# Kernel tuning notes

Measured on AMD Instinct MI355X. Metric: run time of the kernel, lower is better.

The kernel has to match this reference:

```python
import jax, jax.numpy as jnp
import numpy as np

DIM = 512
NUM_HEADS = 8
HEAD_DIM = DIM // NUM_HEADS
GAMMA = 1.0


def setup_inputs() -> dict:
    key = jax.random.key(0)
    ks = jax.random.split(key, 10)
    B, S = 2, 2048
    x_real = jax.random.normal(ks[0], (B, S, DIM), dtype=jnp.float32)
    x_imag = jax.random.normal(ks[1], (B, S, DIM), dtype=jnp.float32)
    def xavier(k, fan_in, fan_out):
        lim = float(np.sqrt(6.0 / (fan_in + fan_out)))
        return jax.random.uniform(k, (fan_in, fan_out), jnp.float32, -lim, lim)
    # torch Linear(in,out): weight [out,in]; we store transposed [in,out]
    Wq = xavier(ks[2], 2 * DIM, DIM); bq = jnp.zeros((DIM,), jnp.float32)
    Wk = xavier(ks[3], 2 * DIM, DIM); bk = jnp.zeros((DIM,), jnp.float32)
    Wv = xavier(ks[4], 2 * DIM, DIM); bv = jnp.zeros((DIM,), jnp.float32)
    Wo = xavier(ks[5], DIM, 2 * DIM); bo = jnp.zeros((2 * DIM,), jnp.float32)
    return {"x_real": x_real, "x_imag": x_imag, "Wq": Wq, "bq": bq,
            "Wk": Wk, "bk": bk, "Wv": Wv, "bv": bv, "Wo": Wo, "bo": bo}


def reference(x_real, x_imag, Wq, bq, Wk, bk, Wv, bv, Wo, bo):
    B, S, _ = x_real.shape
    real_embed = jnp.concatenate([x_real, x_imag], axis=-1)  # [B,S,2*dim]
    def proj(W, b):
        y = real_embed @ W + b                               # [B,S,dim]
        return y.reshape(B, S, NUM_HEADS, HEAD_DIM).transpose(0, 2, 1, 3)  # [B,H,S,d]
    Q = proj(Wq, bq)
    K = proj(Wk, bk)
    V = proj(Wv, bv)
    # softmax over head_dim is broadcast-invariant, so the Bhattacharyya
    # coefficient sum_d sqrt(p_i[d]*q_j[d]) factorizes into a matmul.
    sp = jnp.sqrt(jax.nn.softmax(Q, axis=-1))  # [B,H,S,d]
    sq = jnp.sqrt(jax.nn.softmax(K, axis=-1))  # [B,H,S,d]
    bc = jnp.einsum('bhid,bhjd->bhij', sp, sq)  # Bhattacharyya coeff [B,H,S,S]
    bc = jnp.clip(bc, -1.0, 1.0)
    dist = jnp.arccos(bc)
    attn = jax.nn.softmax(-GAMMA * dist * dist, axis=-1)  # [B,H,S,S]
    attended = jnp.einsum('bhij,bhjd->bhid', attn, V)
    attended = attended.transpose(0, 2, 1, 3).reshape(B, S, DIM)
    out = attended @ Wo + bo  # [B,S,2*dim] = concat(real_out, imag_out)
    return out
```

## Files before the change

kernel.cpp:

```cpp
#include <hip/hip_runtime.h>
#include <math.h>


typedef __attribute__((ext_vector_type(8))) short short8;
typedef __attribute__((ext_vector_type(4))) short bf16x4;
typedef __attribute__((ext_vector_type(4))) float f32x4;
typedef __attribute__((ext_vector_type(2))) float f32x2;
typedef __attribute__((ext_vector_type(4))) unsigned int u32x4;

#define MFMA(a, b, c) __builtin_amdgcn_mfma_f32_16x16x32_bf16((a), (b), (c), 0, 0, 0)

static __device__ __forceinline__ short f2bf(float f) {
    unsigned u = __float_as_uint(f);
    u += 0x7fffu + ((u >> 16) & 1u);
    return (short)(u >> 16);
}

static __device__ __forceinline__ void gld_lds16(const short* g, short* l) {
    __builtin_amdgcn_global_load_lds(
        (const __attribute__((address_space(1))) unsigned int*)g,
        (__attribute__((address_space(3))) unsigned int*)l, 16, 0, 0);
}

__global__ __launch_bounds__(256) void prep_all(
    const float* __restrict__ xr, const float* __restrict__ xi,
    short* __restrict__ xb,
    const float* __restrict__ Wq, const float* __restrict__ Wk,
    const float* __restrict__ Wv, const float* __restrict__ Wo,
    short* __restrict__ wqt, short* __restrict__ wot)
{
    const int bid = blockIdx.x;
    if (bid < 2048) {
        const unsigned wid = bid * 256 + threadIdx.x;
        const int p  = wid & 7;
        const int rp = (wid >> 3) & 31;
        const int kt = (wid >> 8) & 31;
        const int mb = wid >> 13;
        const int up = p ^ (rp & 7);
        const int m  = (mb << 6) | (rp << 1) | (up >> 2);
        const int k  = (kt << 5) | ((up & 3) << 3);
        const float* s = (k < 512) ? (xr + (size_t)m * 512 + k)
                                   : (xi + (size_t)m * 512 + (k - 512));
        float4 t0 = *(const float4*)(s);
        float4 t1 = *(const float4*)(s + 4);
        short8 o;
        o[0] = f2bf(t0.x); o[1] = f2bf(t0.y); o[2] = f2bf(t0.z); o[3] = f2bf(t0.w);
        o[4] = f2bf(t1.x); o[5] = f2bf(t1.y); o[6] = f2bf(t1.z); o[7] = f2bf(t1.w);
        *(short8*)(xb + (size_t)wid * 8) = o;
    } else {
        __shared__ float tt[32][33];
        const int t = bid - 2048;
        const int z = t >> 9;
        const int idx = t & 511;
        const float* src = (z == 0) ? Wq : (z == 1) ? Wk : (z == 2) ? Wv : Wo;
        const int N = (z < 3) ? 512 : 1024;
        const int bx = (z < 3) ? (idx & 15) : (idx & 31);
        const int by = (z < 3) ? (idx >> 4) : (idx >> 5);
        const int n0 = bx << 5, k0 = by << 5;
        const int tx = threadIdx.x & 31, ty = threadIdx.x >> 5;
        #pragma unroll
        for (int i = 0; i < 4; ++i)
            tt[ty + 8 * i][tx] = src[(size_t)(k0 + ty + 8 * i) * N + n0 + tx];
        __syncthreads();
        const int k = k0 + tx;
        const int kt = k >> 5, u = (k >> 3) & 3, off = k & 7;
        #pragma unroll
        for (int i = 0; i < 4; ++i) {
            const int n = n0 + ty + 8 * i;
            const int nb = n >> 6, rn = n & 63;
            const int rp = rn >> 1;
            const int up = ((rn & 1) << 2) | u;
            const int p  = up ^ (rp & 7);
            const float v = tt[tx][ty + 8 * i];
            if (z < 3)
                wqt[(size_t)z * 524288 +
                    ((size_t)(nb * 32 + kt)) * 2048 + rp * 64 + p * 8 + off] = f2bf(v);
            else
                wot[((size_t)(nb * 16 + kt)) * 2048 + rp * 64 + p * 8 + off] = f2bf(v);
        }
    }
}

__global__ __launch_bounds__(64) void qkv_mfma(
    const short* __restrict__ xb, const short* __restrict__ wcat,
    const float* __restrict__ bq, const float* __restrict__ bk,
    const float* __restrict__ bv,
    short* __restrict__ sp, short* __restrict__ sq, short* __restrict__ vt)
{
    __shared__ short As[3][64 * 32];
    __shared__ short Bs[3][64 * 32];
    const int jb = blockIdx.x;
    const int mb = blockIdx.y;
    const int m0 = mb << 6;
    const int lane = threadIdx.x;
    const int l = lane & 15, quad = lane >> 4;
    const int l7 = l & 7;

    const short* gA = xb   + (size_t)mb * 65536 + lane * 8;
    const short* gB = wcat + (size_t)jb * 65536 + lane * 8;

    auto STAGE = [&](int bb, int kk) {
        const int k0 = kk << 11;
        #pragma unroll
        for (int t = 0; t < 4; ++t) {
            gld_lds16(gA + k0 + t * 512, &As[bb][t << 9]);
            gld_lds16(gB + k0 + t * 512, &Bs[bb][t << 9]);
        }
    };

    STAGE(0, 0);
    STAGE(1, 1);
    asm volatile("s_waitcnt vmcnt(8)" ::: "memory");

    const f32x4 z4 = {0.f, 0.f, 0.f, 0.f};
    f32x4 acc[4][4];
    #pragma unroll
    for (int i = 0; i < 4; ++i)
        #pragma unroll
        for (int j = 0; j < 4; ++j) acc[i][j] = z4;

    const int rbase = (l >> 1) << 6;
    const int pA = (((((l & 1) << 2) | quad) ^ ((l >> 1) & 7)) << 3);
    const int rdo = rbase + pA;

    int cb = 0, sb = 2;
    #pragma unroll 1
    for (int kt = 0; kt < 32; ++kt) {
        STAGE(sb, (kt + 2) & 31);
        const short* Al = &As[cb][0];
        const short* Bl = &Bs[cb][0];
        short8 af[4], bfr[4];
        #pragma unroll
        for (int i = 0; i < 4; ++i)
            af[i] = *(const short8*)(Al + (i << 9) + rdo);
        #pragma unroll
        for (int j = 0; j < 4; ++j)
            bfr[j] = *(const short8*)(Bl + (j << 9) + rdo);
        #pragma unroll
        for (int i = 0; i < 4; ++i)
            #pragma unroll
            for (int j = 0; j < 4; ++j)
                acc[i][j] = MFMA(af[i], bfr[j], acc[i][j]);
        asm volatile("s_waitcnt vmcnt(8)" ::: "memory");
        cb = (cb == 2) ? 0 : cb + 1;
        sb = (sb == 2) ? 0 : sb + 1;
    }

    const int op = jb >> 3;
    const int h  = jb & 7;

    if (op < 2) {
        short* dst = (op == 0) ? sp : sq;
        const float* bias = (op == 0) ? bq : bk;
        float bcol[4];
        #pragma unroll
        for (int nt = 0; nt < 4; ++nt) bcol[nt] = bias[(h << 6) + (nt << 4) + l];
        #pragma unroll
        for (int i = 0; i < 4; ++i) {
            #pragma unroll
            for (int reg = 0; reg < 4; ++reg) {
                const int r = m0 + (i << 4) + (quad << 2) + reg;
                const int b = r >> 11, s = r & 2047;
                float v[4];
                #pragma unroll
                for (int nt = 0; nt < 4; ++nt) v[nt] = acc[i][nt][reg] + bcol[nt];
                float mx = fmaxf(fmaxf(v[0], v[1]), fmaxf(v[2], v[3]));
                #pragma unroll
                for (int msk = 1; msk < 16; msk <<= 1) mx = fmaxf(mx, __shfl_xor(mx, msk));
                float e[4], ssum = 0.f;
                #pragma unroll
                for (int nt = 0; nt < 4; ++nt) { e[nt] = __expf(v[nt] - mx); ssum += e[nt]; }
                #pragma unroll
                for (int msk = 1; msk < 16; msk <<= 1) ssum += __shfl_xor(ssum, msk);
                float inv = 1.0f / ssum;
                short* o = dst + ((size_t)((b << 3) + h) * 2048 + s) * 64;
                if (op == 0) {
                    #pragma unroll
                    for (int nt = 0; nt < 4; ++nt)
                        o[(nt << 4) + l] = f2bf(sqrtf(e[nt] * inv));
                } else {
                    const int s7 = r & 7;
                    #pragma unroll
                    for (int nt = 0; nt < 4; ++nt)
                        o[((((nt << 1) + (l >> 3)) ^ s7) << 3) + l7] =
                            f2bf(sqrtf(e[nt] * inv));
                }
            }
        }
    } else {
        float bcol[4];
        #pragma unroll
        for (int nt = 0; nt < 4; ++nt) bcol[nt] = bv[(h << 6) + (nt << 4) + l];
        #pragma unroll
        for (int i = 0; i < 4; ++i) {
            const int sb2 = m0 + (i << 4) + (quad << 2);
            const int b = sb2 >> 11, s = sb2 & 2047;
            const int gg = (s >> 2) & 15;
            const int u = ((gg >> 3) << 2) + (gg & 3);
            const int colp = (s & ~63) + (((u ^ l7)) << 3) + (((gg >> 2) & 1) << 2);
            #pragma unroll
            for (int nt = 0; nt < 4; ++nt) {
                const int d = (nt << 4) + l;
                bf16x4 pk;
                #pragma unroll
                for (int reg = 0; reg < 4; ++reg)
                    pk[reg] = f2bf(acc[i][nt][reg] + bcol[nt]);
                *(bf16x4*)(vt + ((size_t)((b << 3) + h) * 64 + d) * 2048 + colp) = pk;
            }
        }
    }
}

__global__ __launch_bounds__(512, 4) void attn_mfma(
    const short* __restrict__ sp, const short* __restrict__ sq,
    const short* __restrict__ vt,
    float* __restrict__ pnum, float* __restrict__ pden)
{
    __shared__ __align__(16) short sqT[2][64 * 64];
    __shared__ __align__(16) short vtT[2][64 * 64];
    const int bh = blockIdx.y;
    const int m0 = blockIdx.x << 7;
    const int z  = blockIdx.z;
    const int tid = threadIdx.x;
    const int w = tid >> 6, lane = tid & 63;
    const int l = lane & 15, quad = lane >> 4;
    const int l7 = l & 7;

    const short* spB = sp + (size_t)bh * 2048 * 64;
    const short* sqB = sq + (size_t)bh * 2048 * 64;
    const short* vtB = vt + (size_t)bh * 64 * 2048;

    const short* apr = spB + (size_t)(m0 + w * 16 + l) * 64 + quad * 8;
    short8 nq0 = (*(const short8*)(apr)) ^ (short)0x8000;
    short8 nq1 = (*(const short8*)(apr + 32)) ^ (short)0x8000;

    const int lr = lane >> 3;
    const int lu = lane & 7;

    auto STAGEATT = [&](int buf, int jrow) {
        gld_lds16(sqB + (size_t)(jrow + (w << 3) + lr) * 64 + (lu << 3),
                  &sqT[buf][w << 9]);
        gld_lds16(vtB + (size_t)((w << 3) + lr) * 2048 + jrow + (lu << 3),
                  &vtT[buf][w << 9]);
    };

    const int sRd = (quad ^ l7) << 3;

    STAGEATT(0, z << 9);
    __syncthreads();

    const f32x4 ones4 = {1.f, 1.f, 1.f, 1.f};
    const f32x4 z4 = {0.f, 0.f, 0.f, 0.f};
    f32x4 acc[4] = {z4, z4, z4, z4};
    f32x2 den2 = {0.f, 0.f};

    #pragma unroll 1
    for (int jtl = 0; jtl < 8; ++jtl) {
        const int cb = jtl & 1, nb = cb ^ 1;
        const int j0n = ((z << 3) + ((jtl + 1) & 7)) << 6;
        STAGEATT(nb, j0n);

        uint2 pk[4];
        const short* sqL = &sqT[cb][0];
        #pragma unroll
        for (int nt = 0; nt < 4; ++nt) {
            const short* ar = sqL + ((nt * 16 + l) << 6);
            short8 sa0 = *(const short8*)(ar + sRd);
            short8 sa1 = *(const short8*)(ar + (sRd ^ 32));
            f32x4 p = MFMA(sa0, nq0, ones4);
            p = MFMA(sa1, nq1, p);
            f32x2 u01 = {p[0], p[1]};
            f32x2 u23 = {p[2], p[3]};
            const f32x2 zz = {0.f, 0.f};
#if __has_builtin(__builtin_elementwise_max)
            u01 = __builtin_elementwise_max(u01, zz);
            u23 = __builtin_elementwise_max(u23, zz);
#else
            u01.x = fmaxf(u01.x, 0.f); u01.y = fmaxf(u01.y, 0.f);
            u23.x = fmaxf(u23.x, 0.f); u23.y = fmaxf(u23.y, 0.f);
#endif
            f32x2 t01 = {-0.00133017f, -0.00133017f};
            f32x2 t23 = t01;
            t01 = t01 * u01 - 0.00219618f;  t23 = t23 * u23 - 0.00219618f;
            t01 = t01 * u01 - 0.00555151f;  t23 = t23 * u23 - 0.00555151f;
            t01 = t01 * u01 - 0.01465597f;  t23 = t23 * u23 - 0.01465597f;
            t01 = t01 * u01 - 0.04121986f;  t23 = t23 * u23 - 0.04121986f;
            t01 = t01 * u01 - 0.12823956f;  t23 = t23 * u23 - 0.12823956f;
            t01 = t01 * u01 - 0.48089834f;  t23 = t23 * u23 - 0.48089834f;
            t01 = t01 * u01 - 2.88539008f;  t23 = t23 * u23 - 2.88539008f;
            f32x2 w01 = u01 * t01;
            f32x2 w23 = u23 * t23;
#if __has_builtin(__builtin_amdgcn_exp2f)
            float e0 = __builtin_amdgcn_exp2f(w01.x);
            float e1 = __builtin_amdgcn_exp2f(w01.y);
            float e2 = __builtin_amdgcn_exp2f(w23.x);
            float e3 = __builtin_amdgcn_exp2f(w23.y);
#else
            float e0 = exp2f(w01.x), e1 = exp2f(w01.y);
            float e2 = exp2f(w23.x), e3 = exp2f(w23.y);
#endif
            f32x2 es = {e0 + e2, e1 + e3};
            den2 += es;
            pk[nt].x = (__float_as_uint(e0) >> 16) | (__float_as_uint(e1) & 0xffff0000u);
            pk[nt].y = (__float_as_uint(e2) >> 16) | (__float_as_uint(e3) & 0xffff0000u);
        }

        u32x4 c0; c0.x = pk[0].x; c0.y = pk[0].y; c0.z = pk[1].x; c0.w = pk[1].y;
        u32x4 c1; c1.x = pk[2].x; c1.y = pk[2].y; c1.z = pk[3].x; c1.w = pk[3].y;
        short8 pa0 = __builtin_bit_cast(short8, c0);
        short8 pa1 = __builtin_bit_cast(short8, c1);
        const short* vL = &vtT[cb][0];
        #pragma unroll
        for (int t4 = 0; t4 < 4; ++t4) {
            const short* vr = vL + ((t4 * 16 + l) << 6);
            short8 vb0 = *(const short8*)(vr + sRd);
            short8 vb1 = *(const short8*)(vr + (sRd ^ 32));
            acc[t4] = MFMA(pa0, vb0, acc[t4]);
            acc[t4] = MFMA(pa1, vb1, acc[t4]);
        }

        __syncthreads();
    }

    float den = den2.x + den2.y;
    den += __shfl_xor(den, 16);
    den += __shfl_xor(den, 32);
    if (lane < 16)
        pden[(size_t)z * 32768 + bh * 2048 + m0 + w * 16 + l] = den;

    const int b = bh >> 3, hh = bh & 7;
    float* np = pnum + (size_t)z * 4096 * 512;
    #pragma unroll
    for (int t4 = 0; t4 < 4; ++t4)
        #pragma unroll
        for (int reg = 0; reg < 4; ++reg) {
            const int row = m0 + w * 16 + quad * 4 + reg;
            np[((size_t)(b * 2048 + row)) * 512 + hh * 64 + t4 * 16 + l] =
                acc[t4][reg];
        }
}

__global__ __launch_bounds__(256) void combine_attn(
    const float* __restrict__ pnum, const float* __restrict__ pden,
    short* __restrict__ attB)
{
    const int idx = (blockIdx.x * 256 + threadIdx.x) << 3;
    const int r = idx >> 9;
    const int c = idx & 511;
    const int hh = c >> 6;
    const int bh = ((r >> 11) << 3) + hh;
    const int srow = r & 2047;
    float d = 0.f;
    #pragma unroll
    for (int zi = 0; zi < 4; ++zi)
        d += pden[(size_t)zi * 32768 + bh * 2048 + srow];
    const float inv = 1.0f / d;
    float4 a0 = {0.f, 0.f, 0.f, 0.f}, a1 = {0.f, 0.f, 0.f, 0.f};
    #pragma unroll
    for (int zi = 0; zi < 4; ++zi) {
        const float* n0 = pnum + (size_t)zi * 4096 * 512 + (size_t)r * 512 + c;
        float4 b0 = *(const float4*)(n0);
        float4 b1 = *(const float4*)(n0 + 4);
        a0.x += b0.x; a0.y += b0.y; a0.z += b0.z; a0.w += b0.w;
        a1.x += b1.x; a1.y += b1.y; a1.z += b1.z; a1.w += b1.w;
    }
    short8 o;
    o[0] = f2bf(a0.x * inv); o[1] = f2bf(a0.y * inv);
    o[2] = f2bf(a0.z * inv); o[3] = f2bf(a0.w * inv);
    o[4] = f2bf(a1.x * inv); o[5] = f2bf(a1.y * inv);
    o[6] = f2bf(a1.z * inv); o[7] = f2bf(a1.w * inv);
    const int mb = r >> 6, rm = r & 63;
    const int kt = c >> 5, u = (c >> 3) & 3;
    const int rp = rm >> 1;
    const int up = ((rm & 1) << 2) | u;
    const int p  = up ^ (rp & 7);
    *(short8*)(attB + ((size_t)(mb * 16 + kt)) * 2048 + rp * 64 + p * 8) = o;
}

__global__ __launch_bounds__(64) void out_mfma(
    const short* __restrict__ attB, const short* __restrict__ wot,
    const float* __restrict__ bo, float* __restrict__ out)
{
    __shared__ short As[3][64 * 32];
    __shared__ short Bs[3][64 * 32];
    const int nb = blockIdx.x;
    const int mb = blockIdx.y;
    const int n0 = nb << 6;
    const int m0 = mb << 6;
    const int lane = threadIdx.x;
    const int l = lane & 15, quad = lane >> 4;

    const short* gA = attB + (size_t)mb * 32768 + lane * 8;
    const short* gB = wot  + (size_t)nb * 32768 + lane * 8;

    auto STAGE = [&](int bb, int kk) {
        const int k0 = kk << 11;
        #pragma unroll
        for (int t = 0; t < 4; ++t) {
            gld_lds16(gA + k0 + t * 512, &As[bb][t << 9]);
            gld_lds16(gB + k0 + t * 512, &Bs[bb][t << 9]);
        }
    };

    STAGE(0, 0);
    STAGE(1, 1);
    asm volatile("s_waitcnt vmcnt(8)" ::: "memory");

    const f32x4 z4 = {0.f, 0.f, 0.f, 0.f};
    f32x4 acc[4][4];
    #pragma unroll
    for (int i = 0; i < 4; ++i)
        #pragma unroll
        for (int j = 0; j < 4; ++j) acc[i][j] = z4;

    const int rbase = (l >> 1) << 6;
    const int pA = (((((l & 1) << 2) | quad) ^ ((l >> 1) & 7)) << 3);
    const int rdo = rbase + pA;

    int cb = 0, sb = 2;
    #pragma unroll 1
    for (int kt = 0; kt < 16; ++kt) {
        STAGE(sb, (kt + 2) & 15);
        const short* Al = &As[cb][0];
        const short* Bl = &Bs[cb][0];
        short8 af[4], bfr[4];
        #pragma unroll
        for (int i = 0; i < 4; ++i)
            af[i] = *(const short8*)(Al + (i << 9) + rdo);
        #pragma unroll
        for (int j = 0; j < 4; ++j)
            bfr[j] = *(const short8*)(Bl + (j << 9) + rdo);
        #pragma unroll
        for (int i = 0; i < 4; ++i)
            #pragma unroll
            for (int j = 0; j < 4; ++j)
                acc[i][j] = MFMA(af[i], bfr[j], acc[i][j]);
        asm volatile("s_waitcnt vmcnt(8)" ::: "memory");
        cb = (cb == 2) ? 0 : cb + 1;
        sb = (sb == 2) ? 0 : sb + 1;
    }

    float bcol[4];
    #pragma unroll
    for (int nt = 0; nt < 4; ++nt) bcol[nt] = bo[n0 + (nt << 4) + l];
    #pragma unroll
    for (int i = 0; i < 4; ++i)
        #pragma unroll
        for (int reg = 0; reg < 4; ++reg) {
            const int m = m0 + (i << 4) + (quad << 2) + reg;
            float* o = out + (size_t)m * 1024 + n0 + l;
            #pragma unroll
            for (int nt = 0; nt < 4; ++nt)
                o[nt << 4] = acc[i][nt][reg] + bcol[nt];
        }
}

extern "C" void kernel_launch(void* const* d_in, const int* in_sizes, int n_in,
                              void* d_out, int out_size, void* d_ws, size_t ws_size,
                              hipStream_t stream) {
    const float* xr = (const float*)d_in[0];
    const float* xi = (const float*)d_in[1];
    const float* Wq = (const float*)d_in[2];
    const float* bq = (const float*)d_in[3];
    const float* Wk = (const float*)d_in[4];
    const float* bk = (const float*)d_in[5];
    const float* Wv = (const float*)d_in[6];
    const float* bv = (const float*)d_in[7];
    const float* Wo = (const float*)d_in[8];
    const float* bo = (const float*)d_in[9];
    float* out = (float*)d_out;

    short* base = (short*)d_ws;
    short* xb   = base;
    short* wqt  = xb  + 4194304;
    short* wot  = wqt + 1572864;
    short* spW  = wot + 524288;
    short* sqW  = spW + 2097152;
    short* vtW  = sqW + 2097152;
    short* attB = vtW + 2097152;
    float* pnum = (float*)(attB + 2097152);
    float* pden = pnum + 4 * 2097152;

    hipLaunchKernelGGL(prep_all, dim3(4096), dim3(256), 0, stream,
                       xr, xi, xb, Wq, Wk, Wv, Wo, wqt, wot);
    hipLaunchKernelGGL(qkv_mfma, dim3(24, 64), dim3(64), 0, stream,
                       xb, wqt, bq, bk, bv, spW, sqW, vtW);
    hipLaunchKernelGGL(attn_mfma, dim3(16, 16, 4), dim3(512), 0, stream,
                       spW, sqW, vtW, pnum, pden);
    hipLaunchKernelGGL(combine_attn, dim3(1024), dim3(256), 0, stream,
                       pnum, pden, attB);
    hipLaunchKernelGGL(out_mfma, dim3(16, 64), dim3(64), 0, stream,
                       attB, wot, bo, out);
}
```

Before: 183.6 us.

## Drop key-split in attention and fuse normalization into attention epilogue

The attention kernel no longer splits the key dimension across four z-blocks. Each block now loops over all 32 key tiles and divides by its own softmax denominator, kept in shared memory. It writes normalized bf16 output directly in the swizzled layout that the output GEMM expects. This removes the separate combine kernel and the fp32 partial numerator and denominator buffers, which were written and then read back from global memory. In exchange the grid shrinks from 1024 to 256 blocks, so each CU has fewer waves to hide latency, and the epilogue now issues scattered 2-byte stores.

```diff
diff --git a/kernel.cpp b/kernel.cpp
--- a/kernel.cpp
+++ b/kernel.cpp
@@ -213,14 +213,13 @@
 
 __global__ __launch_bounds__(512, 4) void attn_mfma(
     const short* __restrict__ sp, const short* __restrict__ sq,
-    const short* __restrict__ vt,
-    float* __restrict__ pnum, float* __restrict__ pden)
+    const short* __restrict__ vt, short* __restrict__ attB)
 {
     __shared__ __align__(16) short sqT[2][64 * 64];
     __shared__ __align__(16) short vtT[2][64 * 64];
+    __shared__ float denB[8][16];
     const int bh = blockIdx.y;
     const int m0 = blockIdx.x << 7;
-    const int z  = blockIdx.z;
     const int tid = threadIdx.x;
     const int w = tid >> 6, lane = tid & 63;
     const int l = lane & 15, quad = lane >> 4;
@@ -246,7 +245,7 @@
 
     const int sRd = (quad ^ l7) << 3;
 
-    STAGEATT(0, z << 9);
+    STAGEATT(0, 0);
     __syncthreads();
 
     const f32x4 ones4 = {1.f, 1.f, 1.f, 1.f};
@@ -255,9 +254,9 @@
     f32x2 den2 = {0.f, 0.f};
 
     #pragma unroll 1
-    for (int jtl = 0; jtl < 8; ++jtl) {
+    for (int jtl = 0; jtl < 32; ++jtl) {
         const int cb = jtl & 1, nb = cb ^ 1;
-        const int j0n = ((z << 3) + ((jtl + 1) & 7)) << 6;
+        const int j0n = ((jtl + 1) & 31) << 6;
         STAGEATT(nb, j0n);
 
         uint2 pk[4];
@@ -325,56 +324,27 @@
     float den = den2.x + den2.y;
     den += __shfl_xor(den, 16);
     den += __shfl_xor(den, 32);
-    if (lane < 16)
-        pden[(size_t)z * 32768 + bh * 2048 + m0 + w * 16 + l] = den;
+    if (lane < 16) denB[w][l] = den;
+    float invd[4];
+    #pragma unroll
+    for (int reg = 0; reg < 4; ++reg)
+        invd[reg] = 1.0f / denB[w][(quad << 2) + reg];
 
     const int b = bh >> 3, hh = bh & 7;
-    float* np = pnum + (size_t)z * 4096 * 512;
-    #pragma unroll
-    for (int t4 = 0; t4 < 4; ++t4)
+    #pragma unroll
+    for (int t4 = 0; t4 < 4; ++t4) {
+        const int kt = (hh << 1) + (t4 >> 1);
+        const int u = ((t4 << 1) + (l >> 3)) & 3;
         #pragma unroll
         for (int reg = 0; reg < 4; ++reg) {
-            const int row = m0 + w * 16 + quad * 4 + reg;
-            np[((size_t)(b * 2048 + row)) * 512 + hh * 64 + t4 * 16 + l] =
-                acc[t4][reg];
-        }
-}
-
-__global__ __launch_bounds__(256) void combine_attn(
-    const float* __restrict__ pnum, const float* __restrict__ pden,
-    short* __restrict__ attB)
-{
-    const int idx = (blockIdx.x * 256 + threadIdx.x) << 3;
-    const int r = idx >> 9;
-    const int c = idx & 511;
-    const int hh = c >> 6;
-    const int bh = ((r >> 11) << 3) + hh;
-    const int srow = r & 2047;
-    float d = 0.f;
-    #pragma unroll
-    for (int zi = 0; zi < 4; ++zi)
-        d += pden[(size_t)zi * 32768 + bh * 2048 + srow];
-    const float inv = 1.0f / d;
-    float4 a0 = {0.f, 0.f, 0.f, 0.f}, a1 = {0.f, 0.f, 0.f, 0.f};
-    #pragma unroll
-    for (int zi = 0; zi < 4; ++zi) {
-        const float* n0 = pnum + (size_t)zi * 4096 * 512 + (size_t)r * 512 + c;
-        float4 b0 = *(const float4*)(n0);
-        float4 b1 = *(const float4*)(n0 + 4);
-        a0.x += b0.x; a0.y += b0.y; a0.z += b0.z; a0.w += b0.w;
-        a1.x += b1.x; a1.y += b1.y; a1.z += b1.z; a1.w += b1.w;
-    }
-    short8 o;
-    o[0] = f2bf(a0.x * inv); o[1] = f2bf(a0.y * inv);
-    o[2] = f2bf(a0.z * inv); o[3] = f2bf(a0.w * inv);
-    o[4] = f2bf(a1.x * inv); o[5] = f2bf(a1.y * inv);
-    o[6] = f2bf(a1.z * inv); o[7] = f2bf(a1.w * inv);
-    const int mb = r >> 6, rm = r & 63;
-    const int kt = c >> 5, u = (c >> 3) & 3;
-    const int rp = rm >> 1;
-    const int up = ((rm & 1) << 2) | u;
-    const int p  = up ^ (rp & 7);
-    *(short8*)(attB + ((size_t)(mb * 16 + kt)) * 2048 + rp * 64 + p * 8) = o;
+            const int r = (b << 11) + m0 + w * 16 + (quad << 2) + reg;
+            const int mb = r >> 6, rm = r & 63;
+            const int rp = rm >> 1;
+            const int p = (((rm & 1) << 2) | u) ^ (rp & 7);
+            attB[((size_t)(mb * 16 + kt)) * 2048 + rp * 64 + p * 8 + l7] =
+                f2bf(acc[t4][reg] * invd[reg]);
+        }
+    }
 }
 
 __global__ __launch_bounds__(64) void out_mfma(
@@ -478,17 +448,13 @@
     short* sqW  = spW + 2097152;
     short* vtW  = sqW + 2097152;
     short* attB = vtW + 2097152;
-    float* pnum = (float*)(attB + 2097152);
-    float* pden = pnum + 4 * 2097152;
 
     hipLaunchKernelGGL(prep_all, dim3(4096), dim3(256), 0, stream,
                        xr, xi, xb, Wq, Wk, Wv, Wo, wqt, wot);
     hipLaunchKernelGGL(qkv_mfma, dim3(24, 64), dim3(64), 0, stream,
                        xb, wqt, bq, bk, bv, spW, sqW, vtW);
-    hipLaunchKernelGGL(attn_mfma, dim3(16, 16, 4), dim3(512), 0, stream,
-                       spW, sqW, vtW, pnum, pden);
-    hipLaunchKernelGGL(combine_attn, dim3(1024), dim3(256), 0, stream,
-                       pnum, pden, attB);
+    hipLaunchKernelGGL(attn_mfma, dim3(16, 16), dim3(512), 0, stream,
+                       spW, sqW, vtW, attB);
     hipLaunchKernelGGL(out_mfma, dim3(16, 64), dim3(64), 0, stream,
                        attB, wot, bo, out);
 }
```

Result: no change. 184.2 us (+0.3%).
